# Kernel optimization log

Hardware: AMD Instinct MI355X
Metric: run time of the kernel (lower is better)

## Reference

```python
import jax, jax.numpy as jnp
import numpy as np

RES = 8          # voxel_resolution
CLASSES = 40
B, N = 64, 100000


def setup_inputs() -> dict:
    key = jax.random.key(0)
    kx, kw, kb = jax.random.split(key, 3)
    x = jax.random.normal(kx, (B, N, 3), dtype=jnp.float32)
    f = RES ** 3
    # nn.Linear(f, CLASSES): W is (out, in), uniform(-1/sqrt(in), 1/sqrt(in))
    bound = 1.0 / np.sqrt(f)
    W = jax.random.uniform(kw, (CLASSES, f), dtype=jnp.float32, minval=-bound, maxval=bound)
    b = jax.random.uniform(kb, (CLASSES,), dtype=jnp.float32, minval=-bound, maxval=bound)
    return {"x": x, "W": W, "b": b}


def _count_points(x):
    # x: (B, N, 3) -> per-batch adaptive-range 3D histogram, normalized by N
    b_, n_, _ = x.shape
    mins = x.min(axis=1, keepdims=True)            # (B,1,3)
    maxs = x.max(axis=1, keepdims=True)            # (B,1,3)
    rng = maxs - mins
    scale = RES / jnp.where(rng > 0, rng, 1.0)
    # bin index per point per dim; points at max fall in last bin (histogramdd
    # right-closes the final bin) -> clip to RES-1
    idx = jnp.clip(jnp.floor((x - mins) * scale).astype(jnp.int32), 0, RES - 1)  # (B,N,3)
    flat = (idx[..., 0] * RES + idx[..., 1]) * RES + idx[..., 2]                 # (B,N)
    flat = flat + (jnp.arange(b_, dtype=jnp.int32) * (RES ** 3))[:, None]
    counts = jax.ops.segment_sum(
        jnp.ones((b_ * n_,), dtype=x.dtype),
        flat.reshape(-1),
        num_segments=b_ * RES ** 3,
    ).reshape(b_, RES ** 3)
    return counts / n_


def reference(x, W, b):
    counts = _count_points(x)           # (B, RES^3), mode='count'
    logits = counts @ W.T + b           # (B, CLASSES)
    return logits
```

## Files before the change

### kernel.cpp

```cpp
#include <hip/hip_runtime.h>

#define RES 8
#define F 512
#define CLASSES 40
#define B 64
#define NPTS 100000

#define COUNTS_OFF 0
#define MINK_OFF (B * F)
#define MAXK_OFF (B * F + B * 3)

#define MM_BLOCKS 48
#define H_BLOCKS 16

__device__ __forceinline__ unsigned int f2key(float f) {
    unsigned int u = __float_as_uint(f);
    return (u & 0x80000000u) ? ~u : (u | 0x80000000u);
}
__device__ __forceinline__ float key2f(unsigned int k) {
    unsigned int u = (k & 0x80000000u) ? (k ^ 0x80000000u) : ~k;
    return __uint_as_float(u);
}

__global__ __launch_bounds__(256) void init_ws(unsigned int* __restrict__ ws) {
    int i = blockIdx.x * 256 + threadIdx.x;
    if (i < B * F) ws[COUNTS_OFF + i] = 0u;
    if (i < B * 3) {
        ws[MINK_OFF + i] = 0xFFFFFFFFu;
        ws[MAXK_OFF + i] = 0u;
    }
}

__global__ __launch_bounds__(256) void minmax_kernel(const float* __restrict__ x,
                                                     unsigned int* __restrict__ ws) {
    const int batch = blockIdx.y;
    const float4* xb4 = (const float4*)(x + (size_t)batch * (NPTS * 3));
    const int t = threadIdx.x;
    const int NF4 = NPTS * 3 / 4;
    const int stride = MM_BLOCKS * 256;

    float m0 = 3.0e38f, m1 = 3.0e38f, m2 = 3.0e38f;
    float M0 = -3.0e38f, M1 = -3.0e38f, M2 = -3.0e38f;
    for (int i = blockIdx.x * 256 + t; i < NF4; i += stride) {
        float4 e = xb4[i];
        m0 = fminf(m0, fminf(e.x, e.w));  M0 = fmaxf(M0, fmaxf(e.x, e.w));
        m1 = fminf(m1, e.y);              M1 = fmaxf(M1, e.y);
        m2 = fminf(m2, e.z);              M2 = fmaxf(M2, e.z);
    }

    const int c0 = (blockIdx.x * 256 + t) % 3;
    float a0, a1, a2, A0, A1, A2;
    if (c0 == 0)      { a0 = m0; a1 = m1; a2 = m2; A0 = M0; A1 = M1; A2 = M2; }
    else if (c0 == 1) { a0 = m2; a1 = m0; a2 = m1; A0 = M2; A1 = M0; A2 = M1; }
    else              { a0 = m1; a1 = m2; a2 = m0; A0 = M1; A1 = M2; A2 = M0; }

    for (int d = 1; d < 64; d <<= 1) {
        a0 = fminf(a0, __shfl_xor(a0, d)); A0 = fmaxf(A0, __shfl_xor(A0, d));
        a1 = fminf(a1, __shfl_xor(a1, d)); A1 = fmaxf(A1, __shfl_xor(A1, d));
        a2 = fminf(a2, __shfl_xor(a2, d)); A2 = fmaxf(A2, __shfl_xor(A2, d));
    }

    __shared__ float wmin[4][3], wmax[4][3];
    const int wave = t >> 6;
    if ((t & 63) == 0) {
        wmin[wave][0] = a0; wmin[wave][1] = a1; wmin[wave][2] = a2;
        wmax[wave][0] = A0; wmax[wave][1] = A1; wmax[wave][2] = A2;
    }
    __syncthreads();
    if (t < 3) {
        float mn = fminf(fminf(wmin[0][t], wmin[1][t]), fminf(wmin[2][t], wmin[3][t]));
        float mx = fmaxf(fmaxf(wmax[0][t], wmax[1][t]), fmaxf(wmax[2][t], wmax[3][t]));
        atomicMin(&ws[MINK_OFF + batch * 3 + t], f2key(mn));
        atomicMax(&ws[MAXK_OFF + batch * 3 + t], f2key(mx));
    }
}

__global__ __launch_bounds__(256) void hist_kernel(const float* __restrict__ x,
                                                   unsigned int* __restrict__ ws) {
    const int batch = blockIdx.y;
    const int t = threadIdx.x;

    __shared__ unsigned int lh[4][F];
    __shared__ float smn[3], ssc[3];

    for (int i = t; i < 4 * F; i += 256) ((unsigned int*)lh)[i] = 0u;
    if (t < 3) {
        float mn = key2f(ws[MINK_OFF + batch * 3 + t]);
        float mx = key2f(ws[MAXK_OFF + batch * 3 + t]);
        float rng = mx - mn;
        smn[t] = mn;
        ssc[t] = (float)RES / (rng > 0.0f ? rng : 1.0f);
    }
    __syncthreads();

    const float mn0 = smn[0], mn1 = smn[1], mn2 = smn[2];
    const float sc0 = ssc[0], sc1 = ssc[1], sc2 = ssc[2];
    const float4* xb4 = (const float4*)(x + (size_t)batch * (NPTS * 3));
    unsigned int* myh = lh[t >> 6];

    const int NSLOT = NPTS / 4;
    for (int i = blockIdx.x * 256 + t; i < NSLOT; i += H_BLOCKS * 256) {
        float4 p0 = xb4[3 * i + 0];
        float4 p1 = xb4[3 * i + 1];
        float4 p2 = xb4[3 * i + 2];
        float px[4][3] = {{p0.x, p0.y, p0.z},
                          {p0.w, p1.x, p1.y},
                          {p1.z, p1.w, p2.x},
                          {p2.y, p2.z, p2.w}};
#pragma unroll
        for (int q = 0; q < 4; ++q) {
            int i0 = (int)floorf((px[q][0] - mn0) * sc0);
            int i1 = (int)floorf((px[q][1] - mn1) * sc1);
            int i2 = (int)floorf((px[q][2] - mn2) * sc2);
            i0 = min(max(i0, 0), RES - 1);
            i1 = min(max(i1, 0), RES - 1);
            i2 = min(max(i2, 0), RES - 1);
            atomicAdd(&myh[(i0 * RES + i1) * RES + i2], 1u);
        }
    }
    __syncthreads();

    for (int bin = t; bin < F; bin += 256) {
        unsigned int s = lh[0][bin] + lh[1][bin] + lh[2][bin] + lh[3][bin];
        if (s) atomicAdd(&ws[COUNTS_OFF + batch * F + bin], s);
    }
}

__global__ __launch_bounds__(64) void logits_kernel(const unsigned int* __restrict__ ws,
                                                    const float* __restrict__ Wm,
                                                    const float* __restrict__ bias,
                                                    float* __restrict__ out) {
    const int batch = blockIdx.x;
    const int t = threadIdx.x;
    __shared__ float cf[F];
    for (int k = t; k < F; k += 64)
        cf[k] = (float)ws[COUNTS_OFF + batch * F + k] * (1.0f / (float)NPTS);
    __syncthreads();
    if (t < CLASSES) {
        const float4* wr = (const float4*)(Wm + t * F);
        const float4* cf4 = (const float4*)cf;
        float dot = 0.0f;
#pragma unroll 4
        for (int k = 0; k < F / 4; ++k) {
            float4 w = wr[k];
            float4 c = cf4[k];
            dot += c.x * w.x + c.y * w.y + c.z * w.z + c.w * w.w;
        }
        out[batch * CLASSES + t] = dot + bias[t];
    }
}

extern "C" void kernel_launch(void* const* d_in, const int* in_sizes, int n_in,
                              void* d_out, int out_size, void* d_ws, size_t ws_size,
                              hipStream_t stream) {
    const float* x    = (const float*)d_in[0];
    const float* Wm   = (const float*)d_in[1];
    const float* bias = (const float*)d_in[2];
    float* out        = (float*)d_out;
    unsigned int* ws  = (unsigned int*)d_ws;

    init_ws<<<dim3((B * F + 255) / 256), 256, 0, stream>>>(ws);
    minmax_kernel<<<dim3(MM_BLOCKS, B), 256, 0, stream>>>(x, ws);
    hist_kernel<<<dim3(H_BLOCKS, B), 256, 0, stream>>>(x, ws);
    logits_kernel<<<B, 64, 0, stream>>>(ws, Wm, bias, out);
}
```

Baseline: 142.3 us.

## Replace global atomics with per-block partials and drop the init kernel

Min/max and histogram blocks now write per-block partial results to the workspace instead of doing global atomics. The histogram kernel reduces the min/max partials itself, and the logits kernel sums the histogram partials. This removes the init_ws launch and the global atomic traffic. It also doubles the histogram block count, widens the logits block, and splits the dot product into four accumulators, at the cost of extra partial reads in the later kernels.

```diff
diff --git a/kernel.cpp b/kernel.cpp
--- a/kernel.cpp
+++ b/kernel.cpp
@@ -6,30 +6,11 @@
 #define B 64
 #define NPTS 100000
 
-#define COUNTS_OFF 0
-#define MINK_OFF (B * F)
-#define MAXK_OFF (B * F + B * 3)
+#define MM_BLOCKS 48
+#define H_BLOCKS 32
 
-#define MM_BLOCKS 48
-#define H_BLOCKS 16
-
-__device__ __forceinline__ unsigned int f2key(float f) {
-    unsigned int u = __float_as_uint(f);
-    return (u & 0x80000000u) ? ~u : (u | 0x80000000u);
-}
-__device__ __forceinline__ float key2f(unsigned int k) {
-    unsigned int u = (k & 0x80000000u) ? (k ^ 0x80000000u) : ~k;
-    return __uint_as_float(u);
-}
-
-__global__ __launch_bounds__(256) void init_ws(unsigned int* __restrict__ ws) {
-    int i = blockIdx.x * 256 + threadIdx.x;
-    if (i < B * F) ws[COUNTS_OFF + i] = 0u;
-    if (i < B * 3) {
-        ws[MINK_OFF + i] = 0xFFFFFFFFu;
-        ws[MAXK_OFF + i] = 0u;
-    }
-}
+#define PARTH_OFF 0
+#define PARTMM_OFF (B * H_BLOCKS * F)
 
 __global__ __launch_bounds__(256) void minmax_kernel(const float* __restrict__ x,
                                                      unsigned int* __restrict__ ws) {
@@ -70,8 +51,9 @@
     if (t < 3) {
         float mn = fminf(fminf(wmin[0][t], wmin[1][t]), fminf(wmin[2][t], wmin[3][t]));
         float mx = fmaxf(fmaxf(wmax[0][t], wmax[1][t]), fmaxf(wmax[2][t], wmax[3][t]));
-        atomicMin(&ws[MINK_OFF + batch * 3 + t], f2key(mn));
-        atomicMax(&ws[MAXK_OFF + batch * 3 + t], f2key(mx));
+        float* pm = (float*)(ws + PARTMM_OFF) + ((size_t)batch * MM_BLOCKS + blockIdx.x) * 6;
+        pm[t] = mn;
+        pm[3 + t] = mx;
     }
 }
 
@@ -81,12 +63,27 @@
     const int t = threadIdx.x;
 
     __shared__ unsigned int lh[4][F];
+    __shared__ float red[6][16];
     __shared__ float smn[3], ssc[3];
 
     for (int i = t; i < 4 * F; i += 256) ((unsigned int*)lh)[i] = 0u;
+
+    const float* pm = (const float*)(ws + PARTMM_OFF) + (size_t)batch * MM_BLOCKS * 6;
+    if (t < 96) {
+        const int c = t % 6, j0 = t / 6;
+        float v0 = pm[(j0 +  0) * 6 + c];
+        float v1 = pm[(j0 + 16) * 6 + c];
+        float v2 = pm[(j0 + 32) * 6 + c];
+        red[c][j0] = (c < 3) ? fminf(v0, fminf(v1, v2)) : fmaxf(v0, fmaxf(v1, v2));
+    }
+    __syncthreads();
     if (t < 3) {
-        float mn = key2f(ws[MINK_OFF + batch * 3 + t]);
-        float mx = key2f(ws[MAXK_OFF + batch * 3 + t]);
+        float mn = red[t][0], mx = red[t + 3][0];
+#pragma unroll
+        for (int j = 1; j < 16; ++j) {
+            mn = fminf(mn, red[t][j]);
+            mx = fmaxf(mx, red[t + 3][j]);
+        }
         float rng = mx - mn;
         smn[t] = mn;
         ssc[t] = (float)RES / (rng > 0.0f ? rng : 1.0f);
@@ -120,33 +117,42 @@
     }
     __syncthreads();
 
-    for (int bin = t; bin < F; bin += 256) {
-        unsigned int s = lh[0][bin] + lh[1][bin] + lh[2][bin] + lh[3][bin];
-        if (s) atomicAdd(&ws[COUNTS_OFF + batch * F + bin], s);
-    }
+    unsigned int* ph = ws + PARTH_OFF + ((size_t)batch * H_BLOCKS + blockIdx.x) * F;
+    for (int bin = t; bin < F; bin += 256)
+        ph[bin] = lh[0][bin] + lh[1][bin] + lh[2][bin] + lh[3][bin];
 }
 
-__global__ __launch_bounds__(64) void logits_kernel(const unsigned int* __restrict__ ws,
-                                                    const float* __restrict__ Wm,
-                                                    const float* __restrict__ bias,
-                                                    float* __restrict__ out) {
+__global__ __launch_bounds__(256) void logits_kernel(const unsigned int* __restrict__ ws,
+                                                     const float* __restrict__ Wm,
+                                                     const float* __restrict__ bias,
+                                                     float* __restrict__ out) {
     const int batch = blockIdx.x;
     const int t = threadIdx.x;
     __shared__ float cf[F];
-    for (int k = t; k < F; k += 64)
-        cf[k] = (float)ws[COUNTS_OFF + batch * F + k] * (1.0f / (float)NPTS);
+    const unsigned int* ph = ws + PARTH_OFF + (size_t)batch * H_BLOCKS * F;
+    for (int bin = t; bin < F; bin += 256) {
+        unsigned int s = 0;
+#pragma unroll
+        for (int j = 0; j < H_BLOCKS; ++j) s += ph[j * F + bin];
+        cf[bin] = (float)s * (1.0f / (float)NPTS);
+    }
     __syncthreads();
     if (t < CLASSES) {
         const float4* wr = (const float4*)(Wm + t * F);
         const float4* cf4 = (const float4*)cf;
-        float dot = 0.0f;
+        float d0 = 0.f, d1 = 0.f, d2 = 0.f, d3 = 0.f;
 #pragma unroll 4
-        for (int k = 0; k < F / 4; ++k) {
-            float4 w = wr[k];
-            float4 c = cf4[k];
-            dot += c.x * w.x + c.y * w.y + c.z * w.z + c.w * w.w;
+        for (int k = 0; k < F / 4; k += 4) {
+            float4 w0 = wr[k], c0 = cf4[k];
+            float4 w1 = wr[k+1], c1 = cf4[k+1];
+            float4 w2 = wr[k+2], c2 = cf4[k+2];
+            float4 w3 = wr[k+3], c3 = cf4[k+3];
+            d0 += c0.x*w0.x + c0.y*w0.y + c0.z*w0.z + c0.w*w0.w;
+            d1 += c1.x*w1.x + c1.y*w1.y + c1.z*w1.z + c1.w*w1.w;
+            d2 += c2.x*w2.x + c2.y*w2.y + c2.z*w2.z + c2.w*w2.w;
+            d3 += c3.x*w3.x + c3.y*w3.y + c3.z*w3.z + c3.w*w3.w;
         }
-        out[batch * CLASSES + t] = dot + bias[t];
+        out[batch * CLASSES + t] = ((d0 + d1) + (d2 + d3)) + bias[t];
     }
 }
 
@@ -159,8 +165,7 @@
     float* out        = (float*)d_out;
     unsigned int* ws  = (unsigned int*)d_ws;
 
-    init_ws<<<dim3((B * F + 255) / 256), 256, 0, stream>>>(ws);
     minmax_kernel<<<dim3(MM_BLOCKS, B), 256, 0, stream>>>(x, ws);
     hist_kernel<<<dim3(H_BLOCKS, B), 256, 0, stream>>>(x, ws);
-    logits_kernel<<<B, 64, 0, stream>>>(ws, Wm, bias, out);
+    logits_kernel<<<B, 256, 0, stream>>>(ws, Wm, bias, out);
 }
```

Result: faster. 131.4 us (median of 2 runs) (-7.7%).
